# Performance work log

Measured on AMD Instinct MI355X. Metric: run time of the kernel, lower is better.

Reference implementation:

```python
import jax, jax.numpy as jnp
import numpy as np

B, S, D = 4, 2048, 1024
H, DK, DV, DFF = 8, 128, 128, 2048
MASK_VALUE = -1e30
EPS = 1e-14  # K.epsilon()**2 = (1e-7)**2


def setup_inputs() -> dict:
    key = jax.random.key(0)
    ks = jax.random.split(key, 10)
    def g(k, shape, scale=0.02):
        return jax.random.normal(k, shape, dtype=jnp.float32) * scale
    return {
        "query": jax.random.normal(ks[0], (B, S, D), dtype=jnp.float32),
        "key": jax.random.normal(ks[1], (B, S, D), dtype=jnp.float32),
        "value": jax.random.normal(ks[2], (B, S, D), dtype=jnp.float32),
        "mask": jnp.ones((B, S), dtype=jnp.float32),
        "Wq": g(ks[3], (H, D, DK)),
        "Wk": g(ks[4], (H, D, DK)),
        "Wv": g(ks[5], (H, D, DV)),
        "Wo": g(ks[6], (H * DV, D)),
        "W1": g(ks[7], (D, DFF)),
        "b1": jnp.zeros((DFF,), dtype=jnp.float32),
        "W2": g(ks[8], (DFF, D)),
        "b2": jnp.zeros((D,), dtype=jnp.float32),
        "gamma": jnp.ones((2,), dtype=jnp.float32),
        "beta": jnp.zeros((2,), dtype=jnp.float32),
    }


def _layernorm(x, g, b):
    mean = jnp.mean(x, axis=-1, keepdims=True)
    var = jnp.mean(jnp.square(x - mean), axis=-1, keepdims=True)
    return (x - mean) / jnp.sqrt(var + EPS) * g + b


def reference(query, key, value, mask, Wq, Wk, Wv, Wo, W1, b1, W2, b2, gamma, beta):
    # Vectorized over heads (original loops per head; identical math, concat order
    # matches head-major reshape). Note: NO 1/sqrt(dk) scaling in the original.
    q = jnp.einsum('bsd,hdk->bhsk', query, Wq)   # [B,H,S,DK]
    k = jnp.einsum('btd,hdk->bhtk', key, Wk)     # [B,H,S,DK]
    v = jnp.einsum('btd,hdv->bhtv', value, Wv)   # [B,H,S,DV]
    A = jnp.einsum('bhsk,bhtk->bhst', q, k)      # [B,H,S,S]
    m = mask[:, None, None, :]                   # mask over key positions
    A = m * A + (1.0 - m) * MASK_VALUE
    A = jax.nn.softmax(A, axis=-1)
    o = jnp.einsum('bhst,bhtv->bshv', A, v).reshape(query.shape[0], query.shape[1], -1)
    proj = o @ Wo                                # [B,S,D]
    x = _layernorm(value + proj, gamma[0], beta[0])
    ffn = jax.nn.relu(x @ W1 + b1) @ W2 + b2
    x = _layernorm(x + ffn, gamma[1], beta[1])
    return x
```

## Files before the change

kernel.cpp:

```cpp
#include <hip/hip_runtime.h>

#define S_LEN 2048
#define DMODEL 1024
#define NHEAD 8
#define DHEAD 128
#define DFF_N 2048
#define BROWS 8192

typedef unsigned short u16;
typedef __attribute__((ext_vector_type(8))) short bf16x8;
typedef __attribute__((ext_vector_type(4))) float f32x4;
typedef __attribute__((ext_vector_type(16))) float f32x16;

__device__ __forceinline__ u16 f2bf(float f) {
    union { float f; unsigned int u; } v; v.f = f;
    unsigned int u = v.u;
    unsigned int r = (u + 0x7FFFu + ((u >> 16) & 1u)) >> 16;
    return (u16)r;
}

__device__ __forceinline__ void async_copy16(const u16* g, u16* l) {
    __builtin_amdgcn_global_load_lds((const __attribute__((address_space(1))) void*)g,
                                     (__attribute__((address_space(3))) void*)l, 16, 0, 0);
}

__global__ __launch_bounds__(256) void convert3_kernel(const float* __restrict__ a,
                                                       const float* __restrict__ b,
                                                       const float* __restrict__ c,
                                                       u16* __restrict__ oa,
                                                       u16* __restrict__ ob,
                                                       u16* __restrict__ oc, int n4) {
    const float* src = (blockIdx.y == 0) ? a : (blockIdx.y == 1) ? b : c;
    u16* dst = (blockIdx.y == 0) ? oa : (blockIdx.y == 1) ? ob : oc;
    int i = blockIdx.x * 256 + threadIdx.x;
    if (i < n4) {
        float4 v = ((const float4*)src)[i];
        uint2 o;
        o.x = (unsigned)f2bf(v.x) | ((unsigned)f2bf(v.y) << 16);
        o.y = (unsigned)f2bf(v.z) | ((unsigned)f2bf(v.w) << 16);
        ((uint2*)dst)[i] = o;
    }
}

__global__ __launch_bounds__(256) void transpose_bf_tiled(const float* __restrict__ in,
                                                          u16* __restrict__ out,
                                                          int R, int C) {
    __shared__ float T[32][33];
    const long bo = (long)blockIdx.z * R * C;
    const int r0 = blockIdx.y * 32, c0 = blockIdx.x * 32;
    const int tx = threadIdx.x & 31, ty = threadIdx.x >> 5;
    for (int k = 0; k < 4; k++)
        T[ty + 8 * k][tx] = in[bo + (long)(r0 + ty + 8 * k) * C + c0 + tx];
    __syncthreads();
    for (int k = 0; k < 4; k++)
        out[bo + (long)(c0 + ty + 8 * k) * R + r0 + tx] = f2bf(T[tx][ty + 8 * k]);
}

__global__ __launch_bounds__(256) void transpose_qkv_w(const float* __restrict__ Wq,
                                                       const float* __restrict__ Wk,
                                                       const float* __restrict__ Wv,
                                                       u16* __restrict__ WqT,
                                                       u16* __restrict__ WkT,
                                                       u16* __restrict__ WvT) {
    __shared__ float T[32][33];
    const int w = blockIdx.z >> 3, bz = blockIdx.z & 7;
    const float* in = (w == 0) ? Wq : (w == 1) ? Wk : Wv;
    u16* out = (w == 0) ? WqT : (w == 1) ? WkT : WvT;
    const long bo = (long)bz * 1024 * 128;
    const int r0 = blockIdx.y * 32, c0 = blockIdx.x * 32;
    const int tx = threadIdx.x & 31, ty = threadIdx.x >> 5;
    for (int k = 0; k < 4; k++)
        T[ty + 8 * k][tx] = in[bo + (long)(r0 + ty + 8 * k) * 128 + c0 + tx];
    __syncthreads();
    for (int k = 0; k < 4; k++)
        out[bo + (long)(c0 + ty + 8 * k) * 1024 + r0 + tx] = f2bf(T[tx][ty + 8 * k]);
}

__device__ __forceinline__ void gemm_core(const u16* __restrict__ A,
                                          const u16* __restrict__ Bt, int K,
                                          long row0, long col0, u16* As, u16* Bs,
                                          f32x4 (*acc)[4]) {
    const int tid = threadIdx.x;
    const int lane = tid & 63, wave = tid >> 6;
    const int l15 = lane & 15, quad = lane >> 4;
    const int wx = wave & 1, wy = wave >> 1;
    const int srow = wave * 16 + (lane >> 2);
    const int scol = (lane & 3) * 8;
    const u16* ag0 = &A[(row0 + srow) * K + scol];
    const u16* ag1 = &A[(row0 + 64 + srow) * K + scol];
    const u16* bg0 = &Bt[(col0 + srow) * K + scol];
    const u16* bg1 = &Bt[(col0 + 64 + srow) * K + scol];
    const int l0 = (wave * 16) * 32;
    const int l1 = (64 + wave * 16) * 32;
    const int BUF = 128 * 32;

    async_copy16(ag0, &As[l0]);
    async_copy16(ag1, &As[l1]);
    async_copy16(bg0, &Bs[l0]);
    async_copy16(bg1, &Bs[l1]);
    __syncthreads();

    const int nk = K >> 5;
    for (int kt = 0; kt < nk; kt++) {
        const int cur = (kt & 1) * BUF;
        const int nxt = BUF - cur;
        if (kt + 1 < nk) {
            const int k0 = (kt + 1) * 32;
            async_copy16(ag0 + k0, &As[nxt + l0]);
            async_copy16(ag1 + k0, &As[nxt + l1]);
            async_copy16(bg0 + k0, &Bs[nxt + l0]);
            async_copy16(bg1 + k0, &Bs[nxt + l1]);
        }
        bf16x8 af[4], bfr[4];
        for (int mi = 0; mi < 4; mi++)
            af[mi] = *(const bf16x8*)&As[cur + (wy * 64 + mi * 16 + l15) * 32 + quad * 8];
        for (int ni = 0; ni < 4; ni++)
            bfr[ni] = *(const bf16x8*)&Bs[cur + (wx * 64 + ni * 16 + l15) * 32 + quad * 8];
        for (int mi = 0; mi < 4; mi++)
            for (int ni = 0; ni < 4; ni++)
                acc[mi][ni] = __builtin_amdgcn_mfma_f32_16x16x32_bf16(af[mi], bfr[ni],
                                                                      acc[mi][ni], 0, 0, 0);
        __syncthreads();
    }
}

template <int EPI>
__global__ __launch_bounds__(256) void gemm_bt_kernel(const u16* __restrict__ A,
                                                      const u16* __restrict__ Bt,
                                                      const float* __restrict__ bias,
                                                      void* __restrict__ Cp,
                                                      int N, int K) {
    __shared__ u16 As[2 * 128 * 32];
    __shared__ u16 Bs[2 * 128 * 32];
    const int tid = threadIdx.x;
    const int lane = tid & 63, wave = tid >> 6;
    const int l15 = lane & 15, quad = lane >> 4;
    const int wx = wave & 1, wy = wave >> 1;
    const long row0 = (long)blockIdx.x * 128;
    const long col0 = (long)blockIdx.y * 128;

    f32x4 acc[4][4];
    for (int i = 0; i < 4; i++)
        for (int j = 0; j < 4; j++) acc[i][j] = (f32x4){0.f, 0.f, 0.f, 0.f};

    gemm_core(A, Bt, K, row0, col0, As, Bs, acc);

    for (int mi = 0; mi < 4; mi++)
        for (int ni = 0; ni < 4; ni++) {
            const long col = col0 + wx * 64 + ni * 16 + l15;
            float bv = (EPI == 2 || EPI == 3) ? bias[col] : 0.0f;
            for (int r = 0; r < 4; r++) {
                const long row = row0 + wy * 64 + mi * 16 + quad * 4 + r;
                float v = acc[mi][ni][r] + bv;
                if (EPI == 2) v = fmaxf(v, 0.0f);
                if (EPI == 0 || EPI == 3)
                    ((float*)Cp)[row * N + col] = v;
                else
                    ((u16*)Cp)[row * N + col] = f2bf(v);
            }
        }
}

__global__ __launch_bounds__(256) void gemm_qkv_kernel(const u16* __restrict__ A0,
                                                       const u16* __restrict__ A1,
                                                       const u16* __restrict__ A2,
                                                       const u16* __restrict__ B0,
                                                       const u16* __restrict__ B1,
                                                       const u16* __restrict__ B2,
                                                       u16* __restrict__ Qp,
                                                       u16* __restrict__ Kp,
                                                       u16* __restrict__ Vtp) {
    __shared__ u16 As[2 * 128 * 32];
    __shared__ u16 Bs[2 * 128 * 32];
    const int z = blockIdx.z;
    const u16* A = (z == 0) ? A0 : (z == 1) ? A1 : A2;
    const u16* Bt = (z == 0) ? B0 : (z == 1) ? B1 : B2;
    const int tid = threadIdx.x;
    const int lane = tid & 63, wave = tid >> 6;
    const int l15 = lane & 15, quad = lane >> 4;
    const int wx = wave & 1, wy = wave >> 1;
    const long row0 = (long)blockIdx.x * 128;
    const long col0 = (long)blockIdx.y * 128;

    f32x4 acc[4][4];
    for (int i = 0; i < 4; i++)
        for (int j = 0; j < 4; j++) acc[i][j] = (f32x4){0.f, 0.f, 0.f, 0.f};

    gemm_core(A, Bt, 1024, row0, col0, As, Bs, acc);

    if (z == 2) {
        for (int mi = 0; mi < 4; mi++)
            for (int ni = 0; ni < 4; ni++) {
                const int row = (int)row0 + wy * 64 + mi * 16 + quad * 4;
                const int col = (int)col0 + wx * 64 + ni * 16 + l15;
                const int bb = row >> 11, s = row & 2047;
                uint2 o;
                o.x = (unsigned)f2bf(acc[mi][ni][0]) | ((unsigned)f2bf(acc[mi][ni][1]) << 16);
                o.y = (unsigned)f2bf(acc[mi][ni][2]) | ((unsigned)f2bf(acc[mi][ni][3]) << 16);
                *(uint2*)&Vtp[((long)(bb * 1024 + col) << 11) + s] = o;
            }
    } else {
        u16* Cp = (z == 0) ? Qp : Kp;
        for (int mi = 0; mi < 4; mi++)
            for (int ni = 0; ni < 4; ni++) {
                const long col = col0 + wx * 64 + ni * 16 + l15;
                for (int r = 0; r < 4; r++) {
                    const long row = row0 + wy * 64 + mi * 16 + quad * 4 + r;
                    Cp[row * 1024 + col] = f2bf(acc[mi][ni][r]);
                }
            }
    }
}

__global__ __launch_bounds__(256, 2) void attn_kernel(const u16* __restrict__ Q,
                                                      const u16* __restrict__ Km,
                                                      const u16* __restrict__ Vt,
                                                      const float* __restrict__ mask,
                                                      u16* __restrict__ O) {
    __shared__ u16 Kb[2][32 * 128];
    __shared__ u16 Vb[2][128 * 32];
    __shared__ u16 Ps[4][32 * 40];
    const int tid = threadIdx.x;
    const int lane = tid & 63, wave = tid >> 6;
    const int l31 = lane & 31, half = lane >> 5;
    const int b = blockIdx.z, h = blockIdx.y;
    const long baseQ = ((long)b * S_LEN) * DMODEL + h * DHEAD;
    const long baseV = ((long)(b * NHEAD + h) * DHEAD) * S_LEN;
    const int q0 = blockIdx.x * 128 + wave * 32;

    bf16x8 qf[8];
    for (int kk = 0; kk < 8; kk++)
        qf[kk] = *(const bf16x8*)&Q[baseQ + (long)(q0 + l31) * DMODEL + kk * 16 + half * 8];

    const u16* gK[2];
    const u16* gV[2];
    int ldK[2], ldV[2];
    for (int j = 0; j < 2; j++) {
        const int ki = wave + 4 * j;
        const int krow = 4 * ki + (lane >> 4);
        const int kcb = (lane & 15) ^ (krow & 7);
        gK[j] = Km + baseQ + (long)krow * DMODEL + kcb * 8;
        ldK[j] = ki * 512;
        const int vrow = 16 * ki + (lane >> 2);
        const int vcb = (lane & 3) ^ ((vrow >> 1) & 3);
        gV[j] = Vt + baseV + (long)vrow * S_LEN + vcb * 8;
        ldV[j] = ki * 512;
    }

    bf16x8 onesf;
    {
        const short ov = (l31 == 0) ? (short)0x3F80 : (short)0;
        for (int j = 0; j < 8; j++) onesf[j] = ov;
    }

    f32x16 oacc[4], lacc;
    for (int i = 0; i < 4; i++)
        for (int r = 0; r < 16; r++) oacc[i][r] = 0.f;
    for (int r = 0; r < 16; r++) lacc[r] = 0.f;

    for (int j = 0; j < 2; j++) {
        async_copy16(gK[j], &Kb[0][ldK[j]]);
        async_copy16(gV[j], &Vb[0][ldV[j]]);
    }
    __syncthreads();

    const int NKT = S_LEN / 32;
    for (int kt = 0; kt < NKT; kt++) {
        const int cur = kt & 1, nxt = cur ^ 1;
        const float mv = mask[(long)b * S_LEN + kt * 32 + l31];
        if (kt + 1 < NKT) {
            const long off = (long)(kt + 1) * 32;
            for (int j = 0; j < 2; j++) {
                async_copy16(gK[j] + off * DMODEL, &Kb[nxt][ldK[j]]);
                async_copy16(gV[j] + off, &Vb[nxt][ldV[j]]);
            }
        }
        f32x16 st;
        for (int r = 0; r < 16; r++) st[r] = 0.f;
        for (int kk = 0; kk < 8; kk++) {
            bf16x8 kf = *(const bf16x8*)&Kb[cur][l31 * 128 +
                                                 (((kk * 2 + half) ^ (l31 & 7)) * 8)];
            st = __builtin_amdgcn_mfma_f32_32x32x16_bf16(qf[kk], kf, st, 0, 0, 0);
        }
        const float nm = (1.0f - mv) * (-1e30f) - 20.0f;
        for (int r = 0; r < 16; r++) {
            float p = __expf(fmaf(mv, st[r], nm));
            Ps[wave][((r & 3) + 8 * (r >> 2) + 4 * half) * 40 + l31] = f2bf(p);
        }
        asm volatile("s_waitcnt lgkmcnt(0)" ::: "memory");
        for (int kk2 = 0; kk2 < 2; kk2++) {
            bf16x8 pf = *(const bf16x8*)&Ps[wave][l31 * 40 + kk2 * 16 + half * 8];
            for (int nt = 0; nt < 4; nt++) {
                bf16x8 vf = *(const bf16x8*)&Vb[cur][(nt * 32 + l31) * 32 +
                                                     (((kk2 * 2 + half) ^ ((l31 >> 1) & 3)) * 8)];
                oacc[nt] = __builtin_amdgcn_mfma_f32_32x32x16_bf16(pf, vf, oacc[nt], 0, 0, 0);
            }
            lacc = __builtin_amdgcn_mfma_f32_32x32x16_bf16(pf, onesf, lacc, 0, 0, 0);
        }
        __syncthreads();
    }
    float inv[16];
    for (int r = 0; r < 16; r++)
        inv[r] = 1.0f / __shfl(lacc[r], lane & 32, 64);
    for (int nt = 0; nt < 4; nt++)
        for (int r = 0; r < 16; r++) {
            int row = (r & 3) + 8 * (r >> 2) + 4 * half;
            O[baseQ + (long)(q0 + row) * DMODEL + nt * 32 + l31] = f2bf(oacc[nt][r] * inv[r]);
        }
}

__global__ __launch_bounds__(256) void ln_kernel(const float* __restrict__ a,
                                                 const float* __restrict__ b,
                                                 const float* __restrict__ gamma,
                                                 const float* __restrict__ beta, int gi,
                                                 float* __restrict__ out_f,
                                                 u16* __restrict__ out_bf) {
    __shared__ float red[8];
    const int row = blockIdx.x;
    const int tid = threadIdx.x;
    const long off = (long)row * DMODEL + tid * 4;
    float4 va = *(const float4*)&a[off];
    float4 vb = *(const float4*)&b[off];
    float4 v;
    v.x = va.x + vb.x; v.y = va.y + vb.y; v.z = va.z + vb.z; v.w = va.w + vb.w;
    float s = v.x + v.y + v.z + v.w;
    float sq = v.x * v.x + v.y * v.y + v.z * v.z + v.w * v.w;
    for (int d = 1; d < 64; d <<= 1) {
        s += __shfl_xor(s, d, 64);
        sq += __shfl_xor(sq, d, 64);
    }
    int wave = tid >> 6;
    if ((tid & 63) == 0) { red[wave * 2] = s; red[wave * 2 + 1] = sq; }
    __syncthreads();
    s = red[0] + red[2] + red[4] + red[6];
    sq = red[1] + red[3] + red[5] + red[7];
    float mean = s * (1.0f / DMODEL);
    float var = sq * (1.0f / DMODEL) - mean * mean;
    float rstd = rsqrtf(var + 1e-14f);
    float g = gamma[gi], be = beta[gi];
    float4 o;
    o.x = (v.x - mean) * rstd * g + be;
    o.y = (v.y - mean) * rstd * g + be;
    o.z = (v.z - mean) * rstd * g + be;
    o.w = (v.w - mean) * rstd * g + be;
    *(float4*)&out_f[off] = o;
    if (out_bf) {
        uint2 ob;
        ob.x = (unsigned)f2bf(o.x) | ((unsigned)f2bf(o.y) << 16);
        ob.y = (unsigned)f2bf(o.z) | ((unsigned)f2bf(o.w) << 16);
        *(uint2*)&out_bf[off] = ob;
    }
}

extern "C" void kernel_launch(void* const* d_in, const int* in_sizes, int n_in,
                              void* d_out, int out_size, void* d_ws, size_t ws_size,
                              hipStream_t stream) {
    const float* query = (const float*)d_in[0];
    const float* key   = (const float*)d_in[1];
    const float* value = (const float*)d_in[2];
    const float* mask  = (const float*)d_in[3];
    const float* Wq = (const float*)d_in[4];
    const float* Wk = (const float*)d_in[5];
    const float* Wv = (const float*)d_in[6];
    const float* Wo = (const float*)d_in[7];
    const float* W1 = (const float*)d_in[8];
    const float* b1 = (const float*)d_in[9];
    const float* W2 = (const float*)d_in[10];
    const float* b2 = (const float*)d_in[11];
    const float* gamma = (const float*)d_in[12];
    const float* beta  = (const float*)d_in[13];

    char* ws = (char*)d_ws;
    const size_t MB = 1024 * 1024;
    u16* WqT = (u16*)(ws + 0 * MB);
    u16* WkT = (u16*)(ws + 2 * MB);
    u16* WvT = (u16*)(ws + 4 * MB);
    u16* WoT = (u16*)(ws + 6 * MB);
    u16* W1T = (u16*)(ws + 8 * MB);
    u16* W2T = (u16*)(ws + 12 * MB);
    u16* qbf = (u16*)(ws + 16 * MB);
    u16* kbf = (u16*)(ws + 32 * MB);
    u16* vbf = (u16*)(ws + 48 * MB);
    u16* Qp  = (u16*)(ws + 64 * MB);
    u16* Kp  = (u16*)(ws + 80 * MB);
    u16* VtP = (u16*)(ws + 96 * MB);
    u16* Op  = (u16*)(ws + 112 * MB);
    float* proj = (float*)(ws + 128 * MB);
    float* xf   = (float*)(ws + 160 * MB);
    u16* xbf = qbf;
    u16* h1  = kbf;

    transpose_qkv_w<<<dim3(4, 32, 24), 256, 0, stream>>>(Wq, Wk, Wv, WqT, WkT, WvT);
    transpose_bf_tiled<<<dim3(32, 32, 1), 256, 0, stream>>>(Wo, WoT, 1024, 1024);
    transpose_bf_tiled<<<dim3(64, 32, 1), 256, 0, stream>>>(W1, W1T, 1024, 2048);
    transpose_bf_tiled<<<dim3(32, 64, 1), 256, 0, stream>>>(W2, W2T, 2048, 1024);

    const int n4 = BROWS * DMODEL / 4;
    convert3_kernel<<<dim3(n4 / 256, 3), 256, 0, stream>>>(query, key, value, qbf, kbf, vbf, n4);

    gemm_qkv_kernel<<<dim3(64, 8, 3), 256, 0, stream>>>(qbf, kbf, vbf, WqT, WkT, WvT,
                                                        Qp, Kp, VtP);

    attn_kernel<<<dim3(S_LEN / 128, NHEAD, 4), 256, 0, stream>>>(Qp, Kp, VtP, mask, Op);

    gemm_bt_kernel<0><<<dim3(64, 8), 256, 0, stream>>>(Op, WoT, nullptr, proj, 1024, 1024);

    ln_kernel<<<dim3(BROWS), 256, 0, stream>>>(value, proj, gamma, beta, 0, xf, xbf);

    gemm_bt_kernel<2><<<dim3(64, 16), 256, 0, stream>>>(xbf, W1T, b1, h1, 2048, 1024);
    gemm_bt_kernel<3><<<dim3(64, 8), 256, 0, stream>>>(h1, W2T, b2, proj, 1024, 2048);

    ln_kernel<<<dim3(BROWS), 256, 0, stream>>>(xf, proj, gamma, beta, 1, (float*)d_out, nullptr);
}
```

Before: 527.7 us.

## Restructure attention kernel with 64-key tiles and register-resident P fragments

```diff
diff --git a/kernel.cpp b/kernel.cpp
--- a/kernel.cpp
+++ b/kernel.cpp
@@ -22,6 +22,18 @@
 __device__ __forceinline__ void async_copy16(const u16* g, u16* l) {
     __builtin_amdgcn_global_load_lds((const __attribute__((address_space(1))) void*)g,
                                      (__attribute__((address_space(3))) void*)l, 16, 0, 0);
+}
+
+union Frag { bf16x8 v; unsigned u[4]; };
+
+__device__ __forceinline__ unsigned cvt_pk_bf16(float a, float b) {
+    unsigned d;
+    asm("v_cvt_pk_bf16_f32 %0, %1, %2" : "=v"(d) : "v"(a), "v"(b));
+    return d;
+}
+
+__device__ __forceinline__ void pl32swap(unsigned& a, unsigned& b) {
+    asm("v_permlane32_swap_b32 %0, %1" : "+v"(a), "+v"(b));
 }
 
 __global__ __launch_bounds__(256) void convert3_kernel(const float* __restrict__ a,
@@ -217,95 +229,132 @@
                                                       const u16* __restrict__ Vt,
                                                       const float* __restrict__ mask,
                                                       u16* __restrict__ O) {
-    __shared__ u16 Kb[2][32 * 128];
-    __shared__ u16 Vb[2][128 * 32];
-    __shared__ u16 Ps[4][32 * 40];
+    __shared__ u16 Kb[2][64 * 128];
+    __shared__ u16 Vb[2][128 * 64];
     const int tid = threadIdx.x;
     const int lane = tid & 63, wave = tid >> 6;
     const int l31 = lane & 31, half = lane >> 5;
-    const int b = blockIdx.z, h = blockIdx.y;
+
+    const int linear = blockIdx.x;
+    const int xcd = linear & 7, jj = linear >> 3;
+    const int bh = xcd * 4 + (jj & 3);
+    const int qt = jj >> 2;
+    const int b = bh >> 3, h = bh & 7;
+
     const long baseQ = ((long)b * S_LEN) * DMODEL + h * DHEAD;
     const long baseV = ((long)(b * NHEAD + h) * DHEAD) * S_LEN;
-    const int q0 = blockIdx.x * 128 + wave * 32;
+    const int q0 = qt * 128 + wave * 32;
 
     bf16x8 qf[8];
+#pragma unroll
     for (int kk = 0; kk < 8; kk++)
         qf[kk] = *(const bf16x8*)&Q[baseQ + (long)(q0 + l31) * DMODEL + kk * 16 + half * 8];
 
-    const u16* gK[2];
-    const u16* gV[2];
-    int ldK[2], ldV[2];
-    for (int j = 0; j < 2; j++) {
-        const int ki = wave + 4 * j;
-        const int krow = 4 * ki + (lane >> 4);
-        const int kcb = (lane & 15) ^ (krow & 7);
-        gK[j] = Km + baseQ + (long)krow * DMODEL + kcb * 8;
-        ldK[j] = ki * 512;
-        const int vrow = 16 * ki + (lane >> 2);
-        const int vcb = (lane & 3) ^ ((vrow >> 1) & 3);
-        gV[j] = Vt + baseV + (long)vrow * S_LEN + vcb * 8;
-        ldV[j] = ki * 512;
-    }
-
-    bf16x8 onesf;
-    {
-        const short ov = (l31 == 0) ? (short)0x3F80 : (short)0;
-        for (int j = 0; j < 8; j++) onesf[j] = ov;
-    }
-
-    f32x16 oacc[4], lacc;
+    const int krow = 4 * wave + (lane >> 4);
+    const int kcb = (lane & 15) ^ (krow & 7);
+    const u16* gK = Km + baseQ + (long)krow * DMODEL + kcb * 8;
+    const int vrow = 8 * wave + (lane >> 3);
+    const int vcb = (lane & 7) ^ (vrow & 7);
+    const u16* gV = Vt + baseV + (long)vrow * S_LEN + vcb * 8;
+    const int ldo = wave * 512;
+
+    f32x16 oacc[4];
+#pragma unroll
     for (int i = 0; i < 4; i++)
+#pragma unroll
         for (int r = 0; r < 16; r++) oacc[i][r] = 0.f;
-    for (int r = 0; r < 16; r++) lacc[r] = 0.f;
-
-    for (int j = 0; j < 2; j++) {
-        async_copy16(gK[j], &Kb[0][ldK[j]]);
-        async_copy16(gV[j], &Vb[0][ldV[j]]);
+    float lsum = 0.f;
+
+#pragma unroll
+    for (int j = 0; j < 4; j++) {
+        async_copy16(gK + j * (16 * DMODEL), &Kb[0][ldo + j * 2048]);
+        async_copy16(gV + j * (32 * S_LEN), &Vb[0][ldo + j * 2048]);
     }
     __syncthreads();
 
-    const int NKT = S_LEN / 32;
-    for (int kt = 0; kt < NKT; kt++) {
+    const int NT = S_LEN / 64;
+    for (int kt = 0; kt < NT; kt++) {
         const int cur = kt & 1, nxt = cur ^ 1;
-        const float mv = mask[(long)b * S_LEN + kt * 32 + l31];
-        if (kt + 1 < NKT) {
-            const long off = (long)(kt + 1) * 32;
-            for (int j = 0; j < 2; j++) {
-                async_copy16(gK[j] + off * DMODEL, &Kb[nxt][ldK[j]]);
-                async_copy16(gV[j] + off, &Vb[nxt][ldV[j]]);
-            }
-        }
-        f32x16 st;
-        for (int r = 0; r < 16; r++) st[r] = 0.f;
+        if (kt + 1 < NT) {
+            const long koff = (long)(kt + 1) * 64 * DMODEL;
+            const long voff = (long)(kt + 1) * 64;
+#pragma unroll
+            for (int j = 0; j < 4; j++) {
+                async_copy16(gK + koff + j * (16 * DMODEL), &Kb[nxt][ldo + j * 2048]);
+                async_copy16(gV + voff + j * (32 * S_LEN), &Vb[nxt][ldo + j * 2048]);
+            }
+        }
+        const float4* mrow = (const float4*)&mask[(long)b * S_LEN + kt * 64];
+
+        f32x16 st0, st1;
+#pragma unroll
+        for (int r = 0; r < 16; r++) { st0[r] = 0.f; st1[r] = 0.f; }
+        __builtin_amdgcn_s_setprio(1);
+#pragma unroll
         for (int kk = 0; kk < 8; kk++) {
-            bf16x8 kf = *(const bf16x8*)&Kb[cur][l31 * 128 +
-                                                 (((kk * 2 + half) ^ (l31 & 7)) * 8)];
-            st = __builtin_amdgcn_mfma_f32_32x32x16_bf16(qf[kk], kf, st, 0, 0, 0);
-        }
-        const float nm = (1.0f - mv) * (-1e30f) - 20.0f;
+            const int cb = ((kk * 2 + half) ^ (l31 & 7)) * 8;
+            bf16x8 kf0 = *(const bf16x8*)&Kb[cur][l31 * 128 + cb];
+            bf16x8 kf1 = *(const bf16x8*)&Kb[cur][(32 + l31) * 128 + cb];
+            st0 = __builtin_amdgcn_mfma_f32_32x32x16_bf16(kf0, qf[kk], st0, 0, 0, 0);
+            st1 = __builtin_amdgcn_mfma_f32_32x32x16_bf16(kf1, qf[kk], st1, 0, 0, 0);
+        }
+        __builtin_amdgcn_s_setprio(0);
+
+        unsigned dw[8][2];
+#pragma unroll
+        for (int g = 0; g < 4; g++) {
+            const float4 a0 = mrow[2 * g + half];
+            const float4 a1 = mrow[8 + 2 * g + half];
+            const float m0[4] = {a0.x, a0.y, a0.z, a0.w};
+            const float m1[4] = {a1.x, a1.y, a1.z, a1.w};
+            float p0[4], p1[4];
+#pragma unroll
+            for (int jl = 0; jl < 4; jl++) {
+                const int r = 4 * g + jl;
+                p0[jl] = __expf(fmaf(m0[jl], st0[r], fmaf(m0[jl], 1e30f, -1e30f) - 20.0f));
+                p1[jl] = __expf(fmaf(m1[jl], st1[r], fmaf(m1[jl], 1e30f, -1e30f) - 20.0f));
+                lsum += p0[jl] + p1[jl];
+            }
+            dw[g][0] = cvt_pk_bf16(p0[0], p0[1]);
+            dw[g][1] = cvt_pk_bf16(p0[2], p0[3]);
+            dw[4 + g][0] = cvt_pk_bf16(p1[0], p1[1]);
+            dw[4 + g][1] = cvt_pk_bf16(p1[2], p1[3]);
+        }
+        Frag pa[4];
+#pragma unroll
+        for (int f = 0; f < 4; f++)
+#pragma unroll
+            for (int t = 0; t < 2; t++) {
+                unsigned a = dw[2 * f][t], bq = dw[2 * f + 1][t];
+                pl32swap(a, bq);
+                pa[f].u[t] = a;
+                pa[f].u[2 + t] = bq;
+            }
+        __builtin_amdgcn_s_setprio(1);
+#pragma unroll
+        for (int f = 0; f < 4; f++)
+#pragma unroll
+            for (int nt = 0; nt < 4; nt++) {
+                bf16x8 vf = *(const bf16x8*)&Vb[cur][(nt * 32 + l31) * 64 +
+                                                     (((2 * f + half) ^ (l31 & 7)) * 8)];
+                oacc[nt] = __builtin_amdgcn_mfma_f32_32x32x16_bf16(pa[f].v, vf, oacc[nt], 0, 0, 0);
+            }
+        __builtin_amdgcn_s_setprio(0);
+        __syncthreads();
+    }
+
+    lsum += __shfl_xor(lsum, 32, 64);
+    const float invq = 1.0f / lsum;
+    float invv[16];
+#pragma unroll
+    for (int r = 0; r < 16; r++)
+        invv[r] = __shfl(invq, (r & 3) + 8 * (r >> 2) + 4 * half, 64);
+#pragma unroll
+    for (int nt = 0; nt < 4; nt++)
+#pragma unroll
         for (int r = 0; r < 16; r++) {
-            float p = __expf(fmaf(mv, st[r], nm));
-            Ps[wave][((r & 3) + 8 * (r >> 2) + 4 * half) * 40 + l31] = f2bf(p);
-        }
-        asm volatile("s_waitcnt lgkmcnt(0)" ::: "memory");
-        for (int kk2 = 0; kk2 < 2; kk2++) {
-            bf16x8 pf = *(const bf16x8*)&Ps[wave][l31 * 40 + kk2 * 16 + half * 8];
-            for (int nt = 0; nt < 4; nt++) {
-                bf16x8 vf = *(const bf16x8*)&Vb[cur][(nt * 32 + l31) * 32 +
-                                                     (((kk2 * 2 + half) ^ ((l31 >> 1) & 3)) * 8)];
-                oacc[nt] = __builtin_amdgcn_mfma_f32_32x32x16_bf16(pf, vf, oacc[nt], 0, 0, 0);
-            }
-            lacc = __builtin_amdgcn_mfma_f32_32x32x16_bf16(pf, onesf, lacc, 0, 0, 0);
-        }
-        __syncthreads();
-    }
-    float inv[16];
-    for (int r = 0; r < 16; r++)
-        inv[r] = 1.0f / __shfl(lacc[r], lane & 32, 64);
-    for (int nt = 0; nt < 4; nt++)
-        for (int r = 0; r < 16; r++) {
-            int row = (r & 3) + 8 * (r >> 2) + 4 * half;
-            O[baseQ + (long)(q0 + row) * DMODEL + nt * 32 + l31] = f2bf(oacc[nt][r] * inv[r]);
+            const int row = (r & 3) + 8 * (r >> 2) + 4 * half;
+            O[baseQ + (long)(q0 + row) * DMODEL + nt * 32 + l31] = f2bf(oacc[nt][r] * invv[r]);
         }
 }
 
@@ -401,7 +450,7 @@
     gemm_qkv_kernel<<<dim3(64, 8, 3), 256, 0, stream>>>(qbf, kbf, vbf, WqT, WkT, WvT,
                                                         Qp, Kp, VtP);
 
-    attn_kernel<<<dim3(S_LEN / 128, NHEAD, 4), 256, 0, stream>>>(Qp, Kp, VtP, mask, Op);
+    attn_kernel<<<dim3(512, 1, 1), 256, 0, stream>>>(Qp, Kp, VtP, mask, Op);
 
     gemm_bt_kernel<0><<<dim3(64, 8), 256, 0, stream>>>(Op, WoT, nullptr, proj, 1024, 1024);
 
```

Measured after the change: 515.2 us. 2.4% less time.
